# Performance work log

Hardware: AMD Instinct MI355X
Metric: run time of the kernel (lower is better)

## Reference

```python
import jax, jax.numpy as jnp
import numpy as np

B, L, D_MODEL = 2, 1024, 1024
D_STATE, D_CONV, EXPAND, HEADDIM = 64, 4, 2, 64
D_INNER = EXPAND * D_MODEL              # 2048
NHEADS = D_INNER // HEADDIM             # 32
NGROUPS = 1
CONV_DIM = D_INNER + 2 * NGROUPS * D_STATE            # 2176
D_IN_PROJ = 2 * D_INNER + 2 * NGROUPS * D_STATE + NHEADS  # 4256
RMS_EPS = 1e-6      # block nn.RMSNorm eps
GATED_EPS = 1e-5    # Mamba2 RMSNormGated eps

def _rmsnorm(x, w, eps):
    return x * jax.lax.rsqrt(jnp.mean(x * x, axis=-1, keepdims=True) + eps) * w

def _silu(x):
    return x * jax.nn.sigmoid(x)

def _mamba2(x, W_in, conv_w, conv_b, dt_bias, A_log, D_param, ssm_norm_w, W_out):
    b, l, _ = x.shape
    zxbcdt = x @ W_in.T                                   # (b,l,D_IN_PROJ)
    z = zxbcdt[..., :D_INNER]
    xBC = zxbcdt[..., D_INNER:D_INNER + CONV_DIM]
    dt = zxbcdt[..., D_INNER + CONV_DIM:]                 # (b,l,H)
    # depthwise causal conv1d (kernel D_CONV) + silu
    pad = jnp.pad(xBC, ((0, 0), (D_CONV - 1, 0), (0, 0)))
    conv = conv_b + sum(pad[:, i:i + l, :] * conv_w[:, i] for i in range(D_CONV))
    xBC = _silu(conv)
    xs = xBC[..., :D_INNER].reshape(b, l, NHEADS, HEADDIM)
    Bm = xBC[..., D_INNER:D_INNER + D_STATE]              # (b,l,N), ngroups=1
    Cm = xBC[..., D_INNER + D_STATE:]                     # (b,l,N)
    dt = jax.nn.softplus(dt + dt_bias)                    # (b,l,H)
    dA = jnp.exp(dt * (-jnp.exp(A_log)))                  # (b,l,H)
    dtx = dt[..., None] * xs                              # (b,l,H,P)

    def step(h, inp):
        dA_t, dtx_t, B_t, C_t = inp
        h = h * dA_t[:, :, None, None] + dtx_t[..., None] * B_t[:, None, None, :]
        y_t = jnp.einsum('bhpn,bn->bhp', h, C_t)
        return h, y_t

    h0 = jnp.zeros((b, NHEADS, HEADDIM, D_STATE), x.dtype)
    _, ys = jax.lax.scan(step, h0, (dA.transpose(1, 0, 2), dtx.transpose(1, 0, 2, 3),
                                    Bm.transpose(1, 0, 2), Cm.transpose(1, 0, 2)))
    y = ys.transpose(1, 0, 2, 3) + xs * D_param[None, None, :, None]
    y = y.reshape(b, l, D_INNER)
    y = _rmsnorm(y * _silu(z), ssm_norm_w, GATED_EPS)     # RMSNormGated, norm_before_gate=False
    return y @ W_out.T

def _block(x, x_d, norm_w, W_in, conv_w, conv_b, dt_bias, A_log, D_param, ssm_norm_w, W_out, w1, w2):
    # dual_residual=True, residual_scale=1.0, dropout is identity (eval)
    x_ln = _rmsnorm(x, norm_w, RMS_EPS)
    x_f = _mamba2(x_ln, W_in, conv_w, conv_b, dt_bias, A_log, D_param, ssm_norm_w, W_out)
    x_a = x + x_f
    x_f_scaled = x_f
    x_ln = _rmsnorm(x_a, norm_w, RMS_EPS)
    g = x_ln @ w1.T
    x_f = (g * jax.nn.sigmoid(g)) * (x_ln @ w2.T)         # SwiGLU
    x_a = x_a + x_f
    x_f_scaled = x_f_scaled + x_f
    return x_a, x_d + x_f_scaled

def setup_inputs() -> dict:
    key = jax.random.key(0)
    ks = jax.random.split(key, 12)
    dt = jax.random.uniform(ks[6], (NHEADS,), minval=1e-3, maxval=0.1)
    return {
        'x': jax.random.normal(ks[0], (B, L, D_MODEL), jnp.float32),
        'x_d': jax.random.normal(ks[1], (B, L, D_MODEL), jnp.float32),
        'norm_w': jnp.ones((D_MODEL,), jnp.float32),
        'W_in': jax.random.normal(ks[2], (D_IN_PROJ, D_MODEL), jnp.float32) * (D_MODEL ** -0.5),
        'conv_w': jax.random.normal(ks[3], (CONV_DIM, D_CONV), jnp.float32) * 0.2,
        'conv_b': jnp.zeros((CONV_DIM,), jnp.float32),
        'dt_bias': dt + jnp.log(-jnp.expm1(-dt)),   # inverse softplus of dt
        'A_log': jnp.log(jax.random.uniform(ks[7], (NHEADS,), minval=1.0, maxval=16.0)),
        'D_param': jnp.ones((NHEADS,), jnp.float32),
        'ssm_norm_w': jnp.ones((D_INNER,), jnp.float32),
        'W_out': jax.random.normal(ks[4], (D_MODEL, D_INNER), jnp.float32) * (D_INNER ** -0.5),
        'w1': jax.random.normal(ks[8], (D_MODEL, D_MODEL), jnp.float32) * (D_MODEL ** -0.5),
        'w2': jax.random.normal(ks[9], (D_MODEL, D_MODEL), jnp.float32) * (D_MODEL ** -0.5),
    }

def reference(x, x_d, norm_w, W_in, conv_w, conv_b, dt_bias, A_log, D_param, ssm_norm_w, W_out, w1, w2):
    return _block(x, x_d, norm_w, W_in, conv_w, conv_b, dt_bias, A_log, D_param, ssm_norm_w, W_out, w1, w2)
```

## Files before the change

### kernel.cpp

```cpp
#include <hip/hip_runtime.h>

typedef unsigned short u16;
typedef __attribute__((ext_vector_type(8))) short bf16x8;
typedef __attribute__((ext_vector_type(4))) float f32x4;

#define B_      2
#define L_      1024
#define DM      1024
#define DI      2048
#define NH      32
#define HD      64
#define DSTATE  64
#define CONVD   2176
#define DPROJ   4256
#define ZXS     4352

__device__ __forceinline__ u16 f2bf(float f) {
  union { float f; unsigned u; } v; v.f = f;
  unsigned r = v.u + 0x7fffu + ((v.u >> 16) & 1u);
  return (u16)(r >> 16);
}

__device__ __forceinline__ void load_lds16(const void* g, void* l) {
  __builtin_amdgcn_global_load_lds(
      (const __attribute__((address_space(1))) void*)g,
      (__attribute__((address_space(3))) void*)l, 16, 0, 0);
}

template<int P> __device__ __forceinline__ void wait_prefetch() {
  if constexpr (P == 4)      asm volatile("s_waitcnt vmcnt(4)\n\ts_barrier" ::: "memory");
  else if constexpr (P == 6) asm volatile("s_waitcnt vmcnt(6)\n\ts_barrier" ::: "memory");
  else if constexpr (P == 8) asm volatile("s_waitcnt vmcnt(8)\n\ts_barrier" ::: "memory");
}

__device__ __forceinline__ float block_reduce_sum256(float v) {
  #pragma unroll
  for (int off = 32; off > 0; off >>= 1) v += __shfl_down(v, off, 64);
  __shared__ float red[4];
  int lane = threadIdx.x & 63, w = threadIdx.x >> 6;
  if (lane == 0) red[w] = v;
  __syncthreads();
  return red[0] + red[1] + red[2] + red[3];
}

__global__ __launch_bounds__(256) void convert_weights(
    const float* __restrict__ W_in, const float* __restrict__ W_out,
    const float* __restrict__ w1, const float* __restrict__ w2,
    u16* __restrict__ Winb, u16* __restrict__ Woutb, u16* __restrict__ w12b) {
  const long R0 = 4256L * 1024 / 4;
  const long R1 = R0 + 2048L * 1024 / 4;
  long i = (long)blockIdx.x * 256 + threadIdx.x;
  float4 v;
  ushort4* dst;
  if (i < R0) {
    v = ((const float4*)W_in)[i];
    dst = ((ushort4*)Winb) + i;
  } else if (i < R1) {
    long j = i - R0;
    v = ((const float4*)W_out)[j];
    dst = ((ushort4*)Woutb) + j;
  } else {
    long j = i - R1;
    long row = j >> 8;
    const float* s = (row < 1024) ? (w1 + row * 1024) : (w2 + (row - 1024) * 1024);
    v = ((const float4*)s)[j & 255];
    dst = ((ushort4*)w12b) + j;
  }
  *dst = make_ushort4(f2bf(v.x), f2bf(v.y), f2bf(v.z), f2bf(v.w));
}

__global__ __launch_bounds__(256) void add_rms_kernel(
    const float* __restrict__ in1, const float* __restrict__ in2,
    float* __restrict__ sum_out, const float* __restrict__ wt,
    u16* __restrict__ out, float eps) {
  const int row = blockIdx.x;
  const int c = threadIdx.x << 2;
  float4 v = *(const float4*)(in1 + (long)row * DM + c);
  if (in2) {
    float4 u = *(const float4*)(in2 + (long)row * DM + c);
    v.x += u.x; v.y += u.y; v.z += u.z; v.w += u.w;
  }
  if (sum_out) *(float4*)(sum_out + (long)row * DM + c) = v;
  float ss = v.x * v.x + v.y * v.y + v.z * v.z + v.w * v.w;
  float tot = block_reduce_sum256(ss);
  float sc = rsqrtf(tot * (1.0f / DM) + eps);
  float4 wv = *(const float4*)(wt + c);
  *(ushort4*)(out + (long)row * DM + c) =
      make_ushort4(f2bf(v.x * sc * wv.x), f2bf(v.y * sc * wv.y),
                   f2bf(v.z * sc * wv.z), f2bf(v.w * sc * wv.w));
}

template<int NI, int NJ>
__global__ __launch_bounds__(256) void gemm_lds(
    const u16* __restrict__ A, const u16* __restrict__ Bw,
    float* __restrict__ C, int N, int Nw, int K) {
  constexpr int BM = NI * 32;
  constexpr int BN = NJ * 32;
  __shared__ u16 As[2][BM][64];
  __shared__ u16 Bs[2][BN][64];
  const int tid = threadIdx.x;
  const int lane = tid & 63;
  const int wave = tid >> 6;
  const int ml = lane & 15;
  const int quad = lane >> 4;
  const int wm = (wave & 1) * (NI * 16);
  const int wn = (wave >> 1) * (NJ * 16);
  const long bm = (long)blockIdx.y * BM;
  const long bn = (long)blockIdx.x * BN;

  const int lr = lane >> 3;
  const int lc = (lane & 7) ^ lr;

  f32x4 acc[NI][NJ];
  #pragma unroll
  for (int i = 0; i < NI; ++i)
    #pragma unroll
    for (int j = 0; j < NJ; ++j)
      acc[i][j] = (f32x4){0.f, 0.f, 0.f, 0.f};

  auto stage = [&](int kk, int buf) {
    #pragma unroll
    for (int t = 0; t < BM / 32; ++t) {
      const int u = wave * (BM / 32) + t;
      load_lds16(A + (bm + u * 8 + lr) * K + kk + lc * 8, &As[buf][u * 8][0]);
    }
    #pragma unroll
    for (int t = 0; t < BN / 32; ++t) {
      const int u = wave * (BN / 32) + t;
      long brow = bn + u * 8 + lr;
      if (brow >= Nw) brow = Nw - 1;
      load_lds16(Bw + brow * K + kk + lc * 8, &Bs[buf][u * 8][0]);
    }
  };

  stage(0, 0);
  int buf = 0;
  for (int kt = 0; kt < K; kt += 64) {
    if (kt + 64 < K) {
      stage(kt + 64, buf ^ 1);
      wait_prefetch<NI + NJ>();
    } else {
      asm volatile("s_waitcnt vmcnt(0)\n\ts_barrier" ::: "memory");
    }
    #pragma unroll
    for (int ks = 0; ks < 2; ++ks) {
      const int c = ks * 4 + quad;
      const int pc = (c ^ (ml & 7)) << 3;
      bf16x8 af[NI], bfr[NJ];
      #pragma unroll
      for (int i = 0; i < NI; ++i)
        af[i] = *(const bf16x8*)&As[buf][wm + (i << 4) + ml][pc];
      #pragma unroll
      for (int j = 0; j < NJ; ++j)
        bfr[j] = *(const bf16x8*)&Bs[buf][wn + (j << 4) + ml][pc];
      #pragma unroll
      for (int i = 0; i < NI; ++i)
        #pragma unroll
        for (int j = 0; j < NJ; ++j)
          acc[i][j] = __builtin_amdgcn_mfma_f32_16x16x32_bf16(af[i], bfr[j], acc[i][j], 0, 0, 0);
    }
    asm volatile("s_barrier" ::: "memory");
    buf ^= 1;
  }

  const int rquad = quad << 2;
  #pragma unroll
  for (int i = 0; i < NI; ++i) {
    const long gm = bm + wm + (i << 4) + rquad;
    #pragma unroll
    for (int j = 0; j < NJ; ++j) {
      const long gn = bn + wn + (j << 4) + ml;
      #pragma unroll
      for (int r = 0; r < 4; ++r)
        C[(gm + r) * N + gn] = acc[i][j][r];
    }
  }
}

__global__ __launch_bounds__(256) void gemm_mlp_final(
    const u16* __restrict__ A, const u16* __restrict__ Bw,
    const float* __restrict__ xa, const float* __restrict__ xd,
    const float* __restrict__ xf, float* __restrict__ out, int K) {
  __shared__ u16 As[2][64][64];
  __shared__ u16 Bs[2][128][64];
  const int tid = threadIdx.x;
  const int lane = tid & 63;
  const int wave = tid >> 6;
  const int ml = lane & 15;
  const int quad = lane >> 4;
  const int wm = (wave & 1) * 32;
  const int wn = (wave >> 1) * 32;
  const long bm = (long)blockIdx.y * 64;
  const long c0 = (long)blockIdx.x * 64;

  const int lr = lane >> 3;
  const int lc = (lane & 7) ^ lr;

  f32x4 acc[2][4];
  #pragma unroll
  for (int i = 0; i < 2; ++i)
    #pragma unroll
    for (int j = 0; j < 4; ++j)
      acc[i][j] = (f32x4){0.f, 0.f, 0.f, 0.f};

  auto stage = [&](int kk, int buf) {
    #pragma unroll
    for (int t = 0; t < 2; ++t) {
      const int u = wave * 2 + t;
      load_lds16(A + (bm + u * 8 + lr) * K + kk + lc * 8, &As[buf][u * 8][0]);
    }
    #pragma unroll
    for (int t = 0; t < 4; ++t) {
      const int u = wave * 4 + t;
      const int r = u * 8 + lr;
      const long grow = (r < 64) ? (c0 + r) : (1024 + c0 + (r - 64));
      load_lds16(Bw + grow * K + kk + lc * 8, &Bs[buf][u * 8][0]);
    }
  };

  stage(0, 0);
  int buf = 0;
  for (int kt = 0; kt < K; kt += 64) {
    if (kt + 64 < K) {
      stage(kt + 64, buf ^ 1);
      wait_prefetch<6>();
    } else {
      asm volatile("s_waitcnt vmcnt(0)\n\ts_barrier" ::: "memory");
    }
    #pragma unroll
    for (int ks = 0; ks < 2; ++ks) {
      const int c = ks * 4 + quad;
      const int pc = (c ^ (ml & 7)) << 3;
      bf16x8 af[2], bfr[4];
      #pragma unroll
      for (int i = 0; i < 2; ++i)
        af[i] = *(const bf16x8*)&As[buf][wm + (i << 4) + ml][pc];
      #pragma unroll
      for (int j = 0; j < 2; ++j) {
        bfr[j]     = *(const bf16x8*)&Bs[buf][wn + (j << 4) + ml][pc];
        bfr[j + 2] = *(const bf16x8*)&Bs[buf][64 + wn + (j << 4) + ml][pc];
      }
      #pragma unroll
      for (int i = 0; i < 2; ++i)
        #pragma unroll
        for (int j = 0; j < 4; ++j)
          acc[i][j] = __builtin_amdgcn_mfma_f32_16x16x32_bf16(af[i], bfr[j], acc[i][j], 0, 0, 0);
    }
    asm volatile("s_barrier" ::: "memory");
    buf ^= 1;
  }

  float* out1 = out + (long)B_ * L_ * DM;
  const int rquad = quad << 2;
  #pragma unroll
  for (int i = 0; i < 2; ++i) {
    const long gm = bm + wm + (i << 4) + rquad;
    #pragma unroll
    for (int jj = 0; jj < 2; ++jj) {
      const long col = c0 + wn + (jj << 4) + ml;
      #pragma unroll
      for (int r = 0; r < 4; ++r) {
        float g = acc[i][jj][r];
        float h = acc[i][jj + 2][r];
        float e = (g / (1.f + expf(-g))) * h;
        long o = (gm + r) * DM + col;
        out[o]  = xa[o] + e;
        out1[o] = xd[o] + xf[o] + e;
      }
    }
  }
}

__global__ __launch_bounds__(256) void conv_silu_kernel(
    const float* __restrict__ zx, const float* __restrict__ cw,
    const float* __restrict__ cb, float* __restrict__ xc) {
  int idx = blockIdx.x * 256 + threadIdx.x;
  if (idx >= 2048 * 544) return;
  const int c4 = (idx % 544) << 2;
  const int row = idx / 544;
  const int t = row & (L_ - 1);
  float4 acc = *(const float4*)(cb + c4);
  float4 w0 = *(const float4*)(cw + (c4 + 0) * 4);
  float4 w1v = *(const float4*)(cw + (c4 + 1) * 4);
  float4 w2v = *(const float4*)(cw + (c4 + 2) * 4);
  float4 w3v = *(const float4*)(cw + (c4 + 3) * 4);
  const float wts[4][4] = {{w0.x, w0.y, w0.z, w0.w},
                           {w1v.x, w1v.y, w1v.z, w1v.w},
                           {w2v.x, w2v.y, w2v.z, w2v.w},
                           {w3v.x, w3v.y, w3v.z, w3v.w}};
  #pragma unroll
  for (int i = 0; i < 4; ++i) {
    int tau = t - 3 + i;
    if (tau >= 0) {
      float4 xv = *(const float4*)(zx + (long)(row - t + tau) * ZXS + DI + c4);
      acc.x = fmaf(xv.x, wts[0][i], acc.x);
      acc.y = fmaf(xv.y, wts[1][i], acc.y);
      acc.z = fmaf(xv.z, wts[2][i], acc.z);
      acc.w = fmaf(xv.w, wts[3][i], acc.w);
    }
  }
  acc.x = acc.x / (1.f + expf(-acc.x));
  acc.y = acc.y / (1.f + expf(-acc.y));
  acc.z = acc.z / (1.f + expf(-acc.z));
  acc.w = acc.w / (1.f + expf(-acc.w));
  *(float4*)(xc + (long)row * CONVD + c4) = acc;
}

__global__ __launch_bounds__(256) void ssd_chunk_kernel(
    const float* __restrict__ xc, const float* __restrict__ zx,
    const float* __restrict__ dt_bias, const float* __restrict__ A_log,
    float* __restrict__ yss, float* __restrict__ Sbuf,
    float* __restrict__ EGbuf, float* __restrict__ Lam) {
  const int c = blockIdx.x & 15;
  const int h = (blockIdx.x >> 4) & 31;
  const int b = blockIdx.x >> 9;
  const int bh = b * NH + h;
  const long crow = (long)b * L_ + c * 64;
  const int tid = threadIdx.x, lane = tid & 63, wave = tid >> 6;

  __shared__ u16 Cs[64][72], Bs[64][72], Xt[64][72], Btw[64][72], Ms[64][72];
  __shared__ float Gs[64], wjL[64], dtL[64];

  if (wave == 0) {
    float draw = zx[(crow + lane) * ZXS + (DI + CONVD) + h] + dt_bias[h];
    float dt = (draw > 20.f) ? draw : log1pf(expf(draw));
    float g = -expf(A_log[h]) * dt;
    float G = g;
    #pragma unroll
    for (int off = 1; off < 64; off <<= 1) {
      float t = __shfl_up(G, off, 64);
      if (lane >= off) G += t;
    }
    float G63 = __shfl(G, 63, 64);
    Gs[lane] = G;
    wjL[lane] = expf(G63 - G) * dt;
    dtL[lane] = dt;
    EGbuf[(bh * 16 + c) * 64 + lane] = expf(G);
    if (lane == 63) Lam[bh * 16 + c] = expf(G63);
  }
  __syncthreads();
  for (int idx = tid; idx < 1024; idx += 256) {
    int r = idx >> 4, c4 = (idx & 15) << 2;
    const float* row = xc + (crow + r) * CONVD;
    float4 xv = *(const float4*)(row + h * HD + c4);
    Xt[c4 + 0][r] = f2bf(xv.x); Xt[c4 + 1][r] = f2bf(xv.y);
    Xt[c4 + 2][r] = f2bf(xv.z); Xt[c4 + 3][r] = f2bf(xv.w);
    float4 bv = *(const float4*)(row + DI + c4);
    *(ushort4*)&Bs[r][c4] = make_ushort4(f2bf(bv.x), f2bf(bv.y), f2bf(bv.z), f2bf(bv.w));
    float w = wjL[r];
    Btw[c4 + 0][r] = f2bf(bv.x * w); Btw[c4 + 1][r] = f2bf(bv.y * w);
    Btw[c4 + 2][r] = f2bf(bv.z * w); Btw[c4 + 3][r] = f2bf(bv.w * w);
    float4 cv = *(const float4*)(row + DI + DSTATE + c4);
    *(ushort4*)&Cs[r][c4] = make_ushort4(f2bf(cv.x), f2bf(cv.y), f2bf(cv.z), f2bf(cv.w));
  }
  __syncthreads();

  const int mrow = wave * 16 + (lane & 15);
  const int quad = lane >> 4;
  f32x4 accE[4];
  #pragma unroll
  for (int j = 0; j < 4; ++j) accE[j] = (f32x4){0.f, 0.f, 0.f, 0.f};
  #pragma unroll
  for (int ks = 0; ks < 2; ++ks) {
    int k0 = ks * 32 + quad * 8;
    bf16x8 a = *(const bf16x8*)&Cs[mrow][k0];
    #pragma unroll
    for (int j = 0; j < 4; ++j) {
      bf16x8 bfr = *(const bf16x8*)&Bs[j * 16 + (lane & 15)][k0];
      accE[j] = __builtin_amdgcn_mfma_f32_16x16x32_bf16(a, bfr, accE[j], 0, 0, 0);
    }
  }
  #pragma unroll
  for (int j = 0; j < 4; ++j) {
    int jc = j * 16 + (lane & 15);
    float Gj = Gs[jc], dtj = dtL[jc];
    #pragma unroll
    for (int r = 0; r < 4; ++r) {
      int ir = wave * 16 + quad * 4 + r;
      float v = (ir >= jc) ? accE[j][r] * expf(Gs[ir] - Gj) * dtj : 0.f;
      Ms[ir][jc] = f2bf(v);
    }
  }
  __syncthreads();
  f32x4 accY[4], accS[4];
  #pragma unroll
  for (int j = 0; j < 4; ++j) { accY[j] = (f32x4){0.f,0.f,0.f,0.f}; accS[j] = (f32x4){0.f,0.f,0.f,0.f}; }
  #pragma unroll
  for (int ks = 0; ks < 2; ++ks) {
    int k0 = ks * 32 + quad * 8;
    bf16x8 aM = *(const bf16x8*)&Ms[mrow][k0];
    bf16x8 aX = *(const bf16x8*)&Xt[mrow][k0];
    #pragma unroll
    for (int j = 0; j < 4; ++j) {
      bf16x8 bX = *(const bf16x8*)&Xt[j * 16 + (lane & 15)][k0];
      bf16x8 bB = *(const bf16x8*)&Btw[j * 16 + (lane & 15)][k0];
      accY[j] = __builtin_amdgcn_mfma_f32_16x16x32_bf16(aM, bX, accY[j], 0, 0, 0);
      accS[j] = __builtin_amdgcn_mfma_f32_16x16x32_bf16(aX, bB, accS[j], 0, 0, 0);
    }
  }
  float* Sc = Sbuf + (long)(bh * 16 + c) * 4096;
  #pragma unroll
  for (int j = 0; j < 4; ++j) {
    int col = j * 16 + (lane & 15);
    #pragma unroll
    for (int r = 0; r < 4; ++r) {
      int mr = wave * 16 + quad * 4 + r;
      yss[(crow + mr) * DI + h * HD + col] = accY[j][r];
      Sc[mr * 64 + col] = accS[j][r];
    }
  }
}

__global__ __launch_bounds__(256) void ssd_combine_kernel(
    float* __restrict__ Sbuf, const float* __restrict__ Lam) {
  const int bh = blockIdx.x >> 4;
  const int e = (blockIdx.x & 15) * 256 + threadIdx.x;
  float* base = Sbuf + (long)bh * 16 * 4096 + e;
  const float* lamp = Lam + bh * 16;
  float H = 0.f;
  for (int cc = 0; cc < 16; ++cc) {
    float lam = lamp[cc];
    float v = base[cc * 4096];
    base[cc * 4096] = H;
    H = fmaf(lam, H, v);
  }
}

__global__ __launch_bounds__(256) void ssd_final_kernel(
    const float* __restrict__ xc, const float* __restrict__ Sbuf,
    const float* __restrict__ EGbuf, const float* __restrict__ Dp,
    float* __restrict__ yss) {
  const int c = blockIdx.x & 15;
  const int h = (blockIdx.x >> 4) & 31;
  const int b = blockIdx.x >> 9;
  const int bh = b * NH + h;
  const long crow = (long)b * L_ + c * 64;
  const int tid = threadIdx.x, lane = tid & 63, wave = tid >> 6;
  __shared__ u16 Csc[64][72], Hs[64][72];
  __shared__ float egL[64];
  if (tid < 64) egL[tid] = EGbuf[(bh * 16 + c) * 64 + tid];
  __syncthreads();
  const float* Sc = Sbuf + (long)(bh * 16 + c) * 4096;
  for (int idx = tid; idx < 1024; idx += 256) {
    int r = idx >> 4, c4 = (idx & 15) << 2;
    float4 hv = *(const float4*)(Sc + r * 64 + c4);
    *(ushort4*)&Hs[r][c4] = make_ushort4(f2bf(hv.x), f2bf(hv.y), f2bf(hv.z), f2bf(hv.w));
    float eg = egL[r];
    float4 cv = *(const float4*)(xc + (crow + r) * CONVD + DI + DSTATE + c4);
    *(ushort4*)&Csc[r][c4] = make_ushort4(f2bf(cv.x * eg), f2bf(cv.y * eg),
                                          f2bf(cv.z * eg), f2bf(cv.w * eg));
  }
  __syncthreads();
  const int mrow = wave * 16 + (lane & 15);
  const int quad = lane >> 4;
  f32x4 acc[4];
  #pragma unroll
  for (int j = 0; j < 4; ++j) acc[j] = (f32x4){0.f, 0.f, 0.f, 0.f};
  #pragma unroll
  for (int ks = 0; ks < 2; ++ks) {
    int k0 = ks * 32 + quad * 8;
    bf16x8 a = *(const bf16x8*)&Csc[mrow][k0];
    #pragma unroll
    for (int j = 0; j < 4; ++j) {
      bf16x8 bfr = *(const bf16x8*)&Hs[j * 16 + (lane & 15)][k0];
      acc[j] = __builtin_amdgcn_mfma_f32_16x16x32_bf16(a, bfr, acc[j], 0, 0, 0);
    }
  }
  const float Dh = Dp[h];
  #pragma unroll
  for (int j = 0; j < 4; ++j) {
    int p = j * 16 + (lane & 15);
    #pragma unroll
    for (int r = 0; r < 4; ++r) {
      int ir = wave * 16 + quad * 4 + r;
      long o = (crow + ir) * DI + h * HD + p;
      float xval = xc[(crow + ir) * CONVD + h * HD + p];
      yss[o] = yss[o] + acc[j][r] + Dh * xval;
    }
  }
}

__global__ __launch_bounds__(256) void gated_rms_kernel(
    const float* __restrict__ y, const float* __restrict__ zx,
    const float* __restrict__ wt, u16* __restrict__ out) {
  const int row = blockIdx.x;
  const int c = threadIdx.x << 3;
  const float* yr = y + (long)row * DI + c;
  const float* zr = zx + (long)row * ZXS + c;
  float v[8];
  float ss = 0.f;
  #pragma unroll
  for (int i = 0; i < 8; i += 4) {
    float4 y4 = *(const float4*)(yr + i);
    float4 z4 = *(const float4*)(zr + i);
    const float zz[4] = {z4.x, z4.y, z4.z, z4.w};
    const float yy[4] = {y4.x, y4.y, y4.z, y4.w};
    #pragma unroll
    for (int j = 0; j < 4; ++j) {
      float sg = zz[j] / (1.f + expf(-zz[j]));
      float val = yy[j] * sg;
      v[i + j] = val;
      ss += val * val;
    }
  }
  float tot = block_reduce_sum256(ss);
  float sc = rsqrtf(tot * (1.0f / DI) + 1e-5f);
  const float* wr = wt + c;
  *(ushort4*)(out + (long)row * DI + c) =
      make_ushort4(f2bf(v[0] * sc * wr[0]), f2bf(v[1] * sc * wr[1]),
                   f2bf(v[2] * sc * wr[2]), f2bf(v[3] * sc * wr[3]));
  *(ushort4*)(out + (long)row * DI + c + 4) =
      make_ushort4(f2bf(v[4] * sc * wr[4]), f2bf(v[5] * sc * wr[5]),
                   f2bf(v[6] * sc * wr[6]), f2bf(v[7] * sc * wr[7]));
}

extern "C" void kernel_launch(void* const* d_in, const int* in_sizes, int n_in,
                              void* d_out, int out_size, void* d_ws, size_t ws_size,
                              hipStream_t stream) {
  const float* x        = (const float*)d_in[0];
  const float* x_d      = (const float*)d_in[1];
  const float* norm_w   = (const float*)d_in[2];
  const float* W_in     = (const float*)d_in[3];
  const float* conv_w   = (const float*)d_in[4];
  const float* conv_b   = (const float*)d_in[5];
  const float* dt_bias  = (const float*)d_in[6];
  const float* A_log    = (const float*)d_in[7];
  const float* D_param  = (const float*)d_in[8];
  const float* ssm_w    = (const float*)d_in[9];
  const float* W_out    = (const float*)d_in[10];
  const float* w1       = (const float*)d_in[11];
  const float* w2       = (const float*)d_in[12];
  float* out = (float*)d_out;

  char* wsc = (char*)d_ws;
  size_t off = 0;
  auto alloc = [&](size_t n) { char* p = wsc + off; off += (n + 255) & ~(size_t)255; return p; };
  float* zx   = (float*)alloc((size_t)2048 * ZXS * 4);
  float* xc   = (float*)alloc((size_t)2048 * 2176 * 4);
  float* yss  = (float*)alloc((size_t)2048 * 2048 * 4);
  float* xf   = (float*)alloc((size_t)2048 * 1024 * 4);
  float* xa   = (float*)alloc((size_t)2048 * 1024 * 4);
  float* Sbuf = (float*)alloc((size_t)64 * 16 * 4096 * 4);
  float* EGbuf= (float*)alloc((size_t)65536 * 4);
  float* Lam  = (float*)alloc((size_t)1024 * 4);
  u16* xlnb   = (u16*)alloc((size_t)2048 * 1024 * 2);
  u16* ygnb   = (u16*)alloc((size_t)2048 * 2048 * 2);
  u16* xln2b  = (u16*)alloc((size_t)2048 * 1024 * 2);
  u16* Winb   = (u16*)alloc((size_t)4256 * 1024 * 2);
  u16* Woutb  = (u16*)alloc((size_t)1024 * 2048 * 2);
  u16* w12b   = (u16*)alloc((size_t)2048 * 1024 * 2);

  convert_weights<<<8352, 256, 0, stream>>>(W_in, W_out, w1, w2, Winb, Woutb, w12b);
  add_rms_kernel<<<2048, 256, 0, stream>>>(x, nullptr, nullptr, norm_w, xlnb, 1e-6f);
  gemm_lds<4, 2><<<dim3(68, 16), 256, 0, stream>>>(xlnb, Winb, zx, ZXS, 4256, 1024);
  conv_silu_kernel<<<(2048 * 544 + 255) / 256, 256, 0, stream>>>(zx, conv_w, conv_b, xc);
  ssd_chunk_kernel<<<1024, 256, 0, stream>>>(xc, zx, dt_bias, A_log, yss, Sbuf, EGbuf, Lam);
  ssd_combine_kernel<<<1024, 256, 0, stream>>>(Sbuf, Lam);
  ssd_final_kernel<<<1024, 256, 0, stream>>>(xc, Sbuf, EGbuf, D_param, yss);
  gated_rms_kernel<<<2048, 256, 0, stream>>>(yss, zx, ssm_w, ygnb);
  gemm_lds<2, 2><<<dim3(16, 32), 256, 0, stream>>>(ygnb, Woutb, xf, 1024, 1024, 2048);
  add_rms_kernel<<<2048, 256, 0, stream>>>(x, xf, xa, norm_w, xln2b, 1e-6f);
  gemm_mlp_final<<<dim3(16, 32), 256, 0, stream>>>(xln2b, w12b, xa, x_d, xf, out, 1024);
}
```

Baseline: 261.5 us.

## Store intermediates in bf16, fuse first RMSNorm into weight conversion, split-K out-proj

The in-projection output, the conv/SiLU output and the SSM output are now stored as bf16 rather than fp32, which roughly halves the memory traffic of the conv, SSD and gated-norm kernels. The first RMSNorm is merged into the weight-conversion launch as extra blocks, removing one kernel launch. The out-projection GEMM uses split-K=2 with atomicAdd into a buffer that the gated-RMS kernel zeroes, doubling the number of blocks. The cost is lower intermediate precision, including a bf16 round trip on the SSM accumulation, and atomic contention on the output buffer.

Result: faster. 255.0 us (-2.5%).

```diff
diff --git a/kernel.cpp b/kernel.cpp
--- a/kernel.cpp
+++ b/kernel.cpp
@@ -20,6 +20,10 @@
   unsigned r = v.u + 0x7fffu + ((v.u >> 16) & 1u);
   return (u16)(r >> 16);
 }
+__device__ __forceinline__ float bf2f(u16 b) {
+  union { unsigned u; float f; } v; v.u = ((unsigned)b) << 16;
+  return v.f;
+}
 
 __device__ __forceinline__ void load_lds16(const void* g, void* l) {
   __builtin_amdgcn_global_load_lds(
@@ -43,13 +47,27 @@
   return red[0] + red[1] + red[2] + red[3];
 }
 
-__global__ __launch_bounds__(256) void convert_weights(
+__global__ __launch_bounds__(256) void rms_and_convert(
+    const float* __restrict__ x, const float* __restrict__ norm_w, u16* __restrict__ xlnb,
     const float* __restrict__ W_in, const float* __restrict__ W_out,
     const float* __restrict__ w1, const float* __restrict__ w2,
     u16* __restrict__ Winb, u16* __restrict__ Woutb, u16* __restrict__ w12b) {
+  if (blockIdx.x < 2048) {
+    const int row = blockIdx.x;
+    const int c = threadIdx.x << 2;
+    float4 v = *(const float4*)(x + (long)row * DM + c);
+    float ss = v.x * v.x + v.y * v.y + v.z * v.z + v.w * v.w;
+    float tot = block_reduce_sum256(ss);
+    float sc = rsqrtf(tot * (1.0f / DM) + 1e-6f);
+    float4 wv = *(const float4*)(norm_w + c);
+    *(ushort4*)(xlnb + (long)row * DM + c) =
+        make_ushort4(f2bf(v.x * sc * wv.x), f2bf(v.y * sc * wv.y),
+                     f2bf(v.z * sc * wv.z), f2bf(v.w * sc * wv.w));
+    return;
+  }
   const long R0 = 4256L * 1024 / 4;
   const long R1 = R0 + 2048L * 1024 / 4;
-  long i = (long)blockIdx.x * 256 + threadIdx.x;
+  long i = (long)(blockIdx.x - 2048) * 256 + threadIdx.x;
   float4 v;
   ushort4* dst;
   if (i < R0) {
@@ -76,11 +94,9 @@
   const int row = blockIdx.x;
   const int c = threadIdx.x << 2;
   float4 v = *(const float4*)(in1 + (long)row * DM + c);
-  if (in2) {
-    float4 u = *(const float4*)(in2 + (long)row * DM + c);
-    v.x += u.x; v.y += u.y; v.z += u.z; v.w += u.w;
-  }
-  if (sum_out) *(float4*)(sum_out + (long)row * DM + c) = v;
+  float4 u = *(const float4*)(in2 + (long)row * DM + c);
+  v.x += u.x; v.y += u.y; v.z += u.z; v.w += u.w;
+  *(float4*)(sum_out + (long)row * DM + c) = v;
   float ss = v.x * v.x + v.y * v.y + v.z * v.z + v.w * v.w;
   float tot = block_reduce_sum256(ss);
   float sc = rsqrtf(tot * (1.0f / DM) + eps);
@@ -90,10 +106,10 @@
                    f2bf(v.z * sc * wv.z), f2bf(v.w * sc * wv.w));
 }
 
-template<int NI, int NJ>
+template<int NI, int NJ, int OUT>
 __global__ __launch_bounds__(256) void gemm_lds(
     const u16* __restrict__ A, const u16* __restrict__ Bw,
-    float* __restrict__ C, int N, int Nw, int K) {
+    void* __restrict__ Cv, int N, int Nw, int Ksub, int Kstride) {
   constexpr int BM = NI * 32;
   constexpr int BN = NJ * 32;
   __shared__ u16 As[2][BM][64];
@@ -107,6 +123,7 @@
   const int wn = (wave >> 1) * (NJ * 16);
   const long bm = (long)blockIdx.y * BM;
   const long bn = (long)blockIdx.x * BN;
+  const long koff = (long)blockIdx.z * Ksub;
 
   const int lr = lane >> 3;
   const int lc = (lane & 7) ^ lr;
@@ -122,21 +139,21 @@
     #pragma unroll
     for (int t = 0; t < BM / 32; ++t) {
       const int u = wave * (BM / 32) + t;
-      load_lds16(A + (bm + u * 8 + lr) * K + kk + lc * 8, &As[buf][u * 8][0]);
+      load_lds16(A + (bm + u * 8 + lr) * Kstride + koff + kk + lc * 8, &As[buf][u * 8][0]);
     }
     #pragma unroll
     for (int t = 0; t < BN / 32; ++t) {
       const int u = wave * (BN / 32) + t;
       long brow = bn + u * 8 + lr;
       if (brow >= Nw) brow = Nw - 1;
-      load_lds16(Bw + brow * K + kk + lc * 8, &Bs[buf][u * 8][0]);
+      load_lds16(Bw + brow * Kstride + koff + kk + lc * 8, &Bs[buf][u * 8][0]);
     }
   };
 
   stage(0, 0);
   int buf = 0;
-  for (int kt = 0; kt < K; kt += 64) {
-    if (kt + 64 < K) {
+  for (int kt = 0; kt < Ksub; kt += 64) {
+    if (kt + 64 < Ksub) {
       stage(kt + 64, buf ^ 1);
       wait_prefetch<NI + NJ>();
     } else {
@@ -171,8 +188,14 @@
     for (int j = 0; j < NJ; ++j) {
       const long gn = bn + wn + (j << 4) + ml;
       #pragma unroll
-      for (int r = 0; r < 4; ++r)
-        C[(gm + r) * N + gn] = acc[i][j][r];
+      for (int r = 0; r < 4; ++r) {
+        if constexpr (OUT == 0)
+          ((float*)Cv)[(gm + r) * N + gn] = acc[i][j][r];
+        else if constexpr (OUT == 1)
+          ((u16*)Cv)[(gm + r) * N + gn] = f2bf(acc[i][j][r]);
+        else
+          atomicAdd(&((float*)Cv)[(gm + r) * N + gn], acc[i][j][r]);
+      }
     }
   }
 }
@@ -272,8 +295,8 @@
 }
 
 __global__ __launch_bounds__(256) void conv_silu_kernel(
-    const float* __restrict__ zx, const float* __restrict__ cw,
-    const float* __restrict__ cb, float* __restrict__ xc) {
+    const u16* __restrict__ zx, const float* __restrict__ cw,
+    const float* __restrict__ cb, u16* __restrict__ xc) {
   int idx = blockIdx.x * 256 + threadIdx.x;
   if (idx >= 2048 * 544) return;
   const int c4 = (idx % 544) << 2;
@@ -292,24 +315,25 @@
   for (int i = 0; i < 4; ++i) {
     int tau = t - 3 + i;
     if (tau >= 0) {
-      float4 xv = *(const float4*)(zx + (long)(row - t + tau) * ZXS + DI + c4);
-      acc.x = fmaf(xv.x, wts[0][i], acc.x);
-      acc.y = fmaf(xv.y, wts[1][i], acc.y);
-      acc.z = fmaf(xv.z, wts[2][i], acc.z);
-      acc.w = fmaf(xv.w, wts[3][i], acc.w);
+      ushort4 xb = *(const ushort4*)(zx + (long)(row - t + tau) * ZXS + DI + c4);
+      acc.x = fmaf(bf2f(xb.x), wts[0][i], acc.x);
+      acc.y = fmaf(bf2f(xb.y), wts[1][i], acc.y);
+      acc.z = fmaf(bf2f(xb.z), wts[2][i], acc.z);
+      acc.w = fmaf(bf2f(xb.w), wts[3][i], acc.w);
     }
   }
   acc.x = acc.x / (1.f + expf(-acc.x));
   acc.y = acc.y / (1.f + expf(-acc.y));
   acc.z = acc.z / (1.f + expf(-acc.z));
   acc.w = acc.w / (1.f + expf(-acc.w));
-  *(float4*)(xc + (long)row * CONVD + c4) = acc;
+  *(ushort4*)(xc + (long)row * CONVD + c4) =
+      make_ushort4(f2bf(acc.x), f2bf(acc.y), f2bf(acc.z), f2bf(acc.w));
 }
 
 __global__ __launch_bounds__(256) void ssd_chunk_kernel(
-    const float* __restrict__ xc, const float* __restrict__ zx,
+    const u16* __restrict__ xc, const u16* __restrict__ zx,
     const float* __restrict__ dt_bias, const float* __restrict__ A_log,
-    float* __restrict__ yss, float* __restrict__ Sbuf,
+    u16* __restrict__ yss, float* __restrict__ Sbuf,
     float* __restrict__ EGbuf, float* __restrict__ Lam) {
   const int c = blockIdx.x & 15;
   const int h = (blockIdx.x >> 4) & 31;
@@ -322,7 +346,7 @@
   __shared__ float Gs[64], wjL[64], dtL[64];
 
   if (wave == 0) {
-    float draw = zx[(crow + lane) * ZXS + (DI + CONVD) + h] + dt_bias[h];
+    float draw = bf2f(zx[(crow + lane) * ZXS + (DI + CONVD) + h]) + dt_bias[h];
     float dt = (draw > 20.f) ? draw : log1pf(expf(draw));
     float g = -expf(A_log[h]) * dt;
     float G = g;
@@ -341,17 +365,16 @@
   __syncthreads();
   for (int idx = tid; idx < 1024; idx += 256) {
     int r = idx >> 4, c4 = (idx & 15) << 2;
-    const float* row = xc + (crow + r) * CONVD;
-    float4 xv = *(const float4*)(row + h * HD + c4);
-    Xt[c4 + 0][r] = f2bf(xv.x); Xt[c4 + 1][r] = f2bf(xv.y);
-    Xt[c4 + 2][r] = f2bf(xv.z); Xt[c4 + 3][r] = f2bf(xv.w);
-    float4 bv = *(const float4*)(row + DI + c4);
-    *(ushort4*)&Bs[r][c4] = make_ushort4(f2bf(bv.x), f2bf(bv.y), f2bf(bv.z), f2bf(bv.w));
+    const u16* row = xc + (crow + r) * CONVD;
+    ushort4 xv = *(const ushort4*)(row + h * HD + c4);
+    Xt[c4 + 0][r] = xv.x; Xt[c4 + 1][r] = xv.y;
+    Xt[c4 + 2][r] = xv.z; Xt[c4 + 3][r] = xv.w;
+    ushort4 bv = *(const ushort4*)(row + DI + c4);
+    *(ushort4*)&Bs[r][c4] = bv;
     float w = wjL[r];
-    Btw[c4 + 0][r] = f2bf(bv.x * w); Btw[c4 + 1][r] = f2bf(bv.y * w);
-    Btw[c4 + 2][r] = f2bf(bv.z * w); Btw[c4 + 3][r] = f2bf(bv.w * w);
-    float4 cv = *(const float4*)(row + DI + DSTATE + c4);
-    *(ushort4*)&Cs[r][c4] = make_ushort4(f2bf(cv.x), f2bf(cv.y), f2bf(cv.z), f2bf(cv.w));
+    Btw[c4 + 0][r] = f2bf(bf2f(bv.x) * w); Btw[c4 + 1][r] = f2bf(bf2f(bv.y) * w);
+    Btw[c4 + 2][r] = f2bf(bf2f(bv.z) * w); Btw[c4 + 3][r] = f2bf(bf2f(bv.w) * w);
+    *(ushort4*)&Cs[r][c4] = *(const ushort4*)(row + DI + DSTATE + c4);
   }
   __syncthreads();
 
@@ -405,7 +428,7 @@
     #pragma unroll
     for (int r = 0; r < 4; ++r) {
       int mr = wave * 16 + quad * 4 + r;
-      yss[(crow + mr) * DI + h * HD + col] = accY[j][r];
+      yss[(crow + mr) * DI + h * HD + col] = f2bf(accY[j][r]);
       Sc[mr * 64 + col] = accS[j][r];
     }
   }
@@ -427,9 +450,9 @@
 }
 
 __global__ __launch_bounds__(256) void ssd_final_kernel(
-    const float* __restrict__ xc, const float* __restrict__ Sbuf,
+    const u16* __restrict__ xc, const float* __restrict__ Sbuf,
     const float* __restrict__ EGbuf, const float* __restrict__ Dp,
-    float* __restrict__ yss) {
+    u16* __restrict__ yss) {
   const int c = blockIdx.x & 15;
   const int h = (blockIdx.x >> 4) & 31;
   const int b = blockIdx.x >> 9;
@@ -446,9 +469,9 @@
     float4 hv = *(const float4*)(Sc + r * 64 + c4);
     *(ushort4*)&Hs[r][c4] = make_ushort4(f2bf(hv.x), f2bf(hv.y), f2bf(hv.z), f2bf(hv.w));
     float eg = egL[r];
-    float4 cv = *(const float4*)(xc + (crow + r) * CONVD + DI + DSTATE + c4);
-    *(ushort4*)&Csc[r][c4] = make_ushort4(f2bf(cv.x * eg), f2bf(cv.y * eg),
-                                          f2bf(cv.z * eg), f2bf(cv.w * eg));
+    ushort4 cv = *(const ushort4*)(xc + (crow + r) * CONVD + DI + DSTATE + c4);
+    *(ushort4*)&Csc[r][c4] = make_ushort4(f2bf(bf2f(cv.x) * eg), f2bf(bf2f(cv.y) * eg),
+                                          f2bf(bf2f(cv.z) * eg), f2bf(bf2f(cv.w) * eg));
   }
   __syncthreads();
   const int mrow = wave * 16 + (lane & 15);
@@ -474,27 +497,29 @@
     for (int r = 0; r < 4; ++r) {
       int ir = wave * 16 + quad * 4 + r;
       long o = (crow + ir) * DI + h * HD + p;
-      float xval = xc[(crow + ir) * CONVD + h * HD + p];
-      yss[o] = yss[o] + acc[j][r] + Dh * xval;
+      float xval = bf2f(xc[(crow + ir) * CONVD + h * HD + p]);
+      yss[o] = f2bf(bf2f(yss[o]) + acc[j][r] + Dh * xval);
     }
   }
 }
 
 __global__ __launch_bounds__(256) void gated_rms_kernel(
-    const float* __restrict__ y, const float* __restrict__ zx,
-    const float* __restrict__ wt, u16* __restrict__ out) {
+    const u16* __restrict__ y, const u16* __restrict__ zx,
+    const float* __restrict__ wt, u16* __restrict__ out,
+    float* __restrict__ xf_zero) {
   const int row = blockIdx.x;
   const int c = threadIdx.x << 3;
-  const float* yr = y + (long)row * DI + c;
-  const float* zr = zx + (long)row * ZXS + c;
+  const u16* yr = y + (long)row * DI + c;
+  const u16* zr = zx + (long)row * ZXS + c;
+  *(float4*)(xf_zero + (long)row * DM + (threadIdx.x << 2)) = make_float4(0.f, 0.f, 0.f, 0.f);
   float v[8];
   float ss = 0.f;
   #pragma unroll
   for (int i = 0; i < 8; i += 4) {
-    float4 y4 = *(const float4*)(yr + i);
-    float4 z4 = *(const float4*)(zr + i);
-    const float zz[4] = {z4.x, z4.y, z4.z, z4.w};
-    const float yy[4] = {y4.x, y4.y, y4.z, y4.w};
+    ushort4 y4 = *(const ushort4*)(yr + i);
+    ushort4 z4 = *(const ushort4*)(zr + i);
+    const float zz[4] = {bf2f(z4.x), bf2f(z4.y), bf2f(z4.z), bf2f(z4.w)};
+    const float yy[4] = {bf2f(y4.x), bf2f(y4.y), bf2f(y4.z), bf2f(y4.w)};
     #pragma unroll
     for (int j = 0; j < 4; ++j) {
       float sg = zz[j] / (1.f + expf(-zz[j]));
@@ -535,9 +560,9 @@
   char* wsc = (char*)d_ws;
   size_t off = 0;
   auto alloc = [&](size_t n) { char* p = wsc + off; off += (n + 255) & ~(size_t)255; return p; };
-  float* zx   = (float*)alloc((size_t)2048 * ZXS * 4);
-  float* xc   = (float*)alloc((size_t)2048 * 2176 * 4);
-  float* yss  = (float*)alloc((size_t)2048 * 2048 * 4);
+  u16*   zx   = (u16*)alloc((size_t)2048 * ZXS * 2);
+  u16*   xc   = (u16*)alloc((size_t)2048 * 2176 * 2);
+  u16*   yss  = (u16*)alloc((size_t)2048 * 2048 * 2);
   float* xf   = (float*)alloc((size_t)2048 * 1024 * 4);
   float* xa   = (float*)alloc((size_t)2048 * 1024 * 4);
   float* Sbuf = (float*)alloc((size_t)64 * 16 * 4096 * 4);
@@ -550,15 +575,15 @@
   u16* Woutb  = (u16*)alloc((size_t)1024 * 2048 * 2);
   u16* w12b   = (u16*)alloc((size_t)2048 * 1024 * 2);
 
-  convert_weights<<<8352, 256, 0, stream>>>(W_in, W_out, w1, w2, Winb, Woutb, w12b);
-  add_rms_kernel<<<2048, 256, 0, stream>>>(x, nullptr, nullptr, norm_w, xlnb, 1e-6f);
-  gemm_lds<4, 2><<<dim3(68, 16), 256, 0, stream>>>(xlnb, Winb, zx, ZXS, 4256, 1024);
+  rms_and_convert<<<2048 + 8352, 256, 0, stream>>>(x, norm_w, xlnb,
+      W_in, W_out, w1, w2, Winb, Woutb, w12b);
+  gemm_lds<4, 2, 1><<<dim3(68, 16), 256, 0, stream>>>(xlnb, Winb, zx, ZXS, 4256, 1024, 1024);
   conv_silu_kernel<<<(2048 * 544 + 255) / 256, 256, 0, stream>>>(zx, conv_w, conv_b, xc);
   ssd_chunk_kernel<<<1024, 256, 0, stream>>>(xc, zx, dt_bias, A_log, yss, Sbuf, EGbuf, Lam);
   ssd_combine_kernel<<<1024, 256, 0, stream>>>(Sbuf, Lam);
   ssd_final_kernel<<<1024, 256, 0, stream>>>(xc, Sbuf, EGbuf, D_param, yss);
-  gated_rms_kernel<<<2048, 256, 0, stream>>>(yss, zx, ssm_w, ygnb);
-  gemm_lds<2, 2><<<dim3(16, 32), 256, 0, stream>>>(ygnb, Woutb, xf, 1024, 1024, 2048);
+  gated_rms_kernel<<<2048, 256, 0, stream>>>(yss, zx, ssm_w, ygnb, xf);
+  gemm_lds<2, 2, 2><<<dim3(16, 32, 2), 256, 0, stream>>>(ygnb, Woutb, xf, 1024, 1024, 1024, 2048);
   add_rms_kernel<<<2048, 256, 0, stream>>>(x, xf, xa, norm_w, xln2b, 1e-6f);
   gemm_mlp_final<<<dim3(16, 32), 256, 0, stream>>>(xln2b, w12b, xa, x_d, xf, out, 1024);
 }
```
